# Kernel tuning notes

Measured on AMD Instinct MI355X. Metric: run time of the kernel, lower is better.

Reference implementation:

```python
import jax, jax.numpy as jnp
import numpy as np

B, T, D = 4, 4096, 1024


def setup_inputs() -> dict:
    key = jax.random.key(0)
    ks = jax.random.split(key, 7)
    s_in = 1.0 / np.sqrt(D)
    return {
        "x": jax.random.normal(ks[0], (B, T, D), dtype=jnp.float32),
        "W_in": jax.random.uniform(ks[1], (D, 2 * D), jnp.float32, -s_in, s_in),
        "b_in": jax.random.uniform(ks[2], (2 * D,), jnp.float32, -s_in, s_in),
        "A": jax.random.normal(ks[3], (D,), dtype=jnp.float32),
        "C": jax.random.normal(ks[4], (D,), dtype=jnp.float32),
        "W_out": jax.random.uniform(ks[5], (D, D), jnp.float32, -s_in, s_in),
        "b_out": jax.random.uniform(ks[6], (D,), jnp.float32, -s_in, s_in),
    }


def _ssm(v, A, C):
    # diagonal linear recurrence: h_t = sigmoid(A) * h_{t-1} + v_t ; y_t = C * h_t
    decay = jax.nn.sigmoid(A)  # (D,)
    vT = jnp.swapaxes(v, 0, 1)  # (T, B, D)

    def step(h, vt):
        h = decay * h + vt
        return h, h

    h0 = jnp.zeros(vT.shape[1:], dtype=v.dtype)
    _, hs = jax.lax.scan(step, h0, vT)  # (T, B, D)
    return jnp.swapaxes(hs, 0, 1) * C  # (B, T, D)


def reference(x, W_in, b_in, A, C, W_out, b_out):
    proj = x @ W_in + b_in  # (B, T, 2D)
    v, gate = jnp.split(proj, 2, axis=-1)
    gate = jax.nn.sigmoid(gate)
    y = gate * _ssm(v, A, C)
    return y @ W_out + b_out
```

## Files before the change

kernel.cpp:

```cpp
#include <hip/hip_runtime.h>
#include <math.h>

#define BDIM 4
#define TDIM 4096
#define DDIM 1024
#define MDIM (BDIM * TDIM)

#define NC  64
#define LCH 64
static_assert(NC * LCH == TDIM, "chunking");

typedef __attribute__((ext_vector_type(8))) short short8;
typedef __attribute__((ext_vector_type(4))) float f32x4;

__device__ __forceinline__ unsigned short f2bf(float f) {
  unsigned int u = __float_as_uint(f);
  unsigned int r = (u + 0x7fffu + ((u >> 16) & 1u)) >> 16;
  return (unsigned short)r;
}
__device__ __forceinline__ float bf2f(unsigned short h) {
  return __uint_as_float(((unsigned int)h) << 16);
}
__device__ __forceinline__ float sigmoidf_(float x) {
  return 1.0f / (1.0f + expf(-x));
}

__global__ __launch_bounds__(256) void prep_x_kernel(const float* __restrict__ x,
                                                     unsigned short* __restrict__ xh,
                                                     int n4) {
  int i = blockIdx.x * 256 + threadIdx.x;
  if (i >= n4) return;
  float4 f = ((const float4*)x)[i];
  ushort4 h;
  h.x = f2bf(f.x);
  h.y = f2bf(f.y);
  h.z = f2bf(f.z);
  h.w = f2bf(f.w);
  ((ushort4*)xh)[i] = h;
}

__global__ __launch_bounds__(256) void wprep_kernel(const float* __restrict__ in,
                                                    unsigned short* __restrict__ oh,
                                                    int K, int N) {
  __shared__ float t[64][65];
  int n0 = blockIdx.x * 64;
  int k0 = blockIdx.y * 64;
#pragma unroll
  for (int i = 0; i < 16; ++i) {
    int idx = i * 256 + threadIdx.x;
    int r = idx >> 6, c = idx & 63;
    t[r][c] = in[(size_t)(k0 + r) * N + (n0 + c)];
  }
  __syncthreads();
#pragma unroll
  for (int i = 0; i < 16; ++i) {
    int idx = i * 256 + threadIdx.x;
    int rn = idx >> 6, ck = idx & 63;
    oh[(size_t)(n0 + rn) * K + (k0 + ck)] = f2bf(t[ck][rn]);
  }
}


#define BARRIER()                                  \
  do {                                             \
    asm volatile("" ::: "memory");                 \
    __builtin_amdgcn_s_barrier();                  \
    asm volatile("" ::: "memory");                 \
  } while (0)

#define RD_A(SET, BK)                                                           \
  _Pragma("unroll") for (int m = 0; m < 4; ++m)                                 \
      SET[m] = *(const short8*)(ldsb + (((BK) ? baseA1 : baseA0) + m * 2048));

#define RD_B(SET, BK)                                                           \
  _Pragma("unroll") for (int n = 0; n < 4; ++n)                                 \
      SET[n] = *(const short8*)(ldsb + 16384 + (((BK) ? baseB1 : baseB0) +      \
                                                n * 2048));

#define MFMA16(ASET, BSET)                                                      \
  _Pragma("unroll") for (int m = 0; m < 4; ++m)                                 \
      _Pragma("unroll") for (int n = 0; n < 4; ++n)                             \
          acc[m][n] = __builtin_amdgcn_mfma_f32_16x16x32_bf16(                  \
              ASET[m], BSET[n], acc[m][n], 0, 0, 0);

#define STAGE(PTR, S, BUFB, KOFF)                                               \
  __builtin_amdgcn_global_load_lds(                                             \
      (const __attribute__((address_space(1))) unsigned int*)((PTR) + off##S +  \
                                                              (KOFF)),          \
      (__attribute__((address_space(3))) unsigned int*)((char*)lds + (BUFB) +   \
                                                        (S) * 4096 +            \
                                                        wave * 1024),           \
      16, 0, 0);

template <int EPI>
__global__ __launch_bounds__(256, 4) void gemm128(const unsigned short* __restrict__ A,
                                                  const unsigned short* __restrict__ B,
                                                  const float* __restrict__ bias,
                                                  float* __restrict__ outF,
                                                  unsigned short* __restrict__ outV,
                                                  unsigned short* __restrict__ outG,
                                                  const float* __restrict__ Adec,
                                                  float* __restrict__ chunkp,
                                                  int nNt, int K) {
  __shared__ unsigned short lds[16384];

  int cpx = gridDim.x >> 3;
  int bid = blockIdx.x;
  int swz = (bid & 7) * cpx + (bid >> 3);
  int mtile = swz / nNt, ntile = swz % nNt;

  int tid = threadIdx.x;
  int wave = tid >> 6, lane = tid & 63;
  int wm = wave >> 1, wn = wave & 1;
  int rA = wm * 64 + (lane & 15);
  int rB = wn * 64 + (lane & 15);
  int kq2 = (lane >> 4) * 16;

  int baseA0 = ((rA << 7) + kq2) ^ ((rA & 7) << 4);
  int baseA1 = ((rA << 7) + kq2 + 64) ^ ((rA & 7) << 4);
  int baseB0 = ((rB << 7) + kq2) ^ ((rB & 7) << 4);
  int baseB1 = ((rB << 7) + kq2 + 64) ^ ((rB & 7) << 4);
  const char* ldsb = (const char*)lds;

#define MKOFF(S) \
  ({ int Lt = (S) * 4096 + tid * 16; int P = Lt ^ (((Lt >> 7) & 7) << 4); \
     ((P >> 7) * (K << 1)) + (P & 127); })
  int off0 = MKOFF(0), off1 = MKOFF(1), off2 = MKOFF(2), off3 = MKOFF(3);
#undef MKOFF

  const char* AgB = (const char*)(A + (size_t)(mtile * 128) * K);
  const char* BgB = (const char*)(B + (size_t)(ntile * 128) * K);

  f32x4 acc[4][4] = {};
  short8 af[4], bf[4];

  int NT = K >> 6;
  for (int t = 0; t < NT; ++t) {
    int k0 = t << 7;
    STAGE(AgB, 0, 0, k0) STAGE(AgB, 1, 0, k0)
    STAGE(AgB, 2, 0, k0) STAGE(AgB, 3, 0, k0)
    STAGE(BgB, 0, 16384, k0) STAGE(BgB, 1, 16384, k0)
    STAGE(BgB, 2, 16384, k0) STAGE(BgB, 3, 16384, k0)
    asm volatile("s_waitcnt vmcnt(0)" ::: "memory");
    BARRIER();
    RD_A(af, 0);
    RD_B(bf, 0);
    MFMA16(af, bf);
    RD_A(af, 1);
    RD_B(bf, 1);
    MFMA16(af, bf);
    BARRIER();
  }

  int q = lane >> 4;
  int row0 = mtile * 128 + wm * 64 + (q << 2);
  int col0 = ntile * 128 + wn * 64 + (lane & 15);

  if (EPI == 0) {
#pragma unroll
    for (int m = 0; m < 4; ++m) {
#pragma unroll
      for (int n = 0; n < 4; ++n) {
        int col = col0 + n * 16;
        float bv = bias[col];
#pragma unroll
        for (int j = 0; j < 4; ++j) {
          int row = row0 + m * 16 + j;
          outF[(size_t)row * (nNt * 128) + col] = acc[m][n][j] + bv;
        }
      }
    }
  } else if (col0 >= DDIM) {
#pragma unroll
    for (int m = 0; m < 4; ++m) {
#pragma unroll
      for (int n = 0; n < 4; ++n) {
        int col = col0 + n * 16;
        float bv = bias[col];
#pragma unroll
        for (int j = 0; j < 4; ++j) {
          int row = row0 + m * 16 + j;
          outG[(size_t)row * DDIM + (col - DDIM)] = f2bf(sigmoidf_(acc[m][n][j] + bv));
        }
      }
    }
  } else {
    float partial[4];
#pragma unroll
    for (int n = 0; n < 4; ++n) {
      int col = col0 + n * 16;
      float bv = bias[col];
      float dec = sigmoidf_(Adec[col]);
      float l2d = __log2f(dec);
      float p = 0.f;
#pragma unroll
      for (int m = 0; m < 4; ++m) {
#pragma unroll
        for (int j = 0; j < 4; ++j) {
          int row = row0 + m * 16 + j;
          unsigned short ush = f2bf(acc[m][n][j] + bv);
          outV[(size_t)row * DDIM + col] = ush;
          float w = exp2f((float)(63 - (q * 4 + m * 16 + j)) * l2d);
          p = fmaf(w, bf2f(ush), p);
        }
      }
      partial[n] = p;
    }
#pragma unroll
    for (int n = 0; n < 4; ++n) {
      partial[n] += __shfl_xor(partial[n], 16, 64);
      partial[n] += __shfl_xor(partial[n], 32, 64);
    }
    if (q == 0) {
      int chunkg = mtile * 2 + wm;
#pragma unroll
      for (int n = 0; n < 4; ++n)
        chunkp[(size_t)chunkg * DDIM + col0 + n * 16] = partial[n];
    }
  }
}

__global__ __launch_bounds__(256) void ssm_phase2(const float* __restrict__ A,
                                                  const float* __restrict__ chunkp,
                                                  float* __restrict__ chunkh) {
  int idx = blockIdx.x * 256 + threadIdx.x;
  int b = idx >> 10, d = idx & 1023;
  float dec = sigmoidf_(A[d]);
  float dL = dec;
#pragma unroll
  for (int i = 0; i < 6; ++i) dL *= dL;
  float hv[NC];
#pragma unroll
  for (int c = 0; c < NC; ++c) hv[c] = chunkp[(size_t)(b * NC + c) * DDIM + d];
  float carry = 0.f;
#pragma unroll
  for (int c = 0; c < NC; ++c) {
    float local = hv[c];
    chunkh[(size_t)(b * NC + c) * DDIM + d] = carry;
    carry = fmaf(dL, carry, local);
  }
}

__global__ __launch_bounds__(256) void ssm_phase3(const unsigned short* __restrict__ v,
                                                  const unsigned short* __restrict__ g,
                                                  const float* __restrict__ A,
                                                  const float* __restrict__ C,
                                                  const float* __restrict__ chunkh,
                                                  unsigned short* __restrict__ ybf) {
  int b = blockIdx.y, c = blockIdx.x;
  int d0 = threadIdx.x * 4;
  float4 a4 = *(const float4*)&A[d0];
  float4 c4 = *(const float4*)&C[d0];
  float dx = sigmoidf_(a4.x), dy = sigmoidf_(a4.y), dz = sigmoidf_(a4.z), dw = sigmoidf_(a4.w);
  float4 h0 = *(const float4*)&chunkh[(size_t)(b * NC + c) * DDIM + d0];
  float hx = h0.x, hy = h0.y, hz = h0.z, hw = h0.w;
  size_t base = ((size_t)b * TDIM + (size_t)c * LCH) * DDIM + d0;
  const ushort4* vp = (const ushort4*)(v + base);
  const ushort4* gp = (const ushort4*)(g + base);
  ushort4* yp = (ushort4*)(ybf + base);
#pragma unroll 4
  for (int i = 0; i < LCH; ++i) {
    ushort4 vv = vp[(size_t)i * (DDIM / 4)];
    ushort4 gg = gp[(size_t)i * (DDIM / 4)];
    hx = fmaf(dx, hx, bf2f(vv.x));
    hy = fmaf(dy, hy, bf2f(vv.y));
    hz = fmaf(dz, hz, bf2f(vv.z));
    hw = fmaf(dw, hw, bf2f(vv.w));
    ushort4 yy;
    yy.x = f2bf(bf2f(gg.x) * c4.x * hx);
    yy.y = f2bf(bf2f(gg.y) * c4.y * hy);
    yy.z = f2bf(bf2f(gg.z) * c4.z * hz);
    yy.w = f2bf(bf2f(gg.w) * c4.w * hw);
    yp[(size_t)i * (DDIM / 4)] = yy;
  }
}

extern "C" void kernel_launch(void* const* d_in, const int* in_sizes, int n_in,
                              void* d_out, int out_size, void* d_ws, size_t ws_size,
                              hipStream_t stream) {
  const float* x = (const float*)d_in[0];
  const float* W_in = (const float*)d_in[1];
  const float* b_in = (const float*)d_in[2];
  const float* A = (const float*)d_in[3];
  const float* C = (const float*)d_in[4];
  const float* W_out = (const float*)d_in[5];
  const float* b_out = (const float*)d_in[6];
  float* out = (float*)d_out;

  char* ws = (char*)d_ws;
  const size_t MK = (size_t)MDIM * DDIM;
  unsigned short* xh = (unsigned short*)ws;    ws += MK * 2;
  unsigned short* winh = (unsigned short*)ws;  ws += (size_t)2 * DDIM * DDIM * 2;
  unsigned short* wouth = (unsigned short*)ws; ws += (size_t)DDIM * DDIM * 2;
  unsigned short* v = (unsigned short*)ws;     ws += MK * 2;
  unsigned short* g = (unsigned short*)ws;     ws += MK * 2;
  unsigned short* ybf = (unsigned short*)ws;   ws += MK * 2;
  float* chunkp = (float*)ws;                  ws += (size_t)BDIM * NC * DDIM * 4;
  float* chunkh = (float*)ws;                  ws += (size_t)BDIM * NC * DDIM * 4;

  prep_x_kernel<<<(int)(MK / 4 / 256), 256, 0, stream>>>(x, xh, (int)(MK / 4));
  wprep_kernel<<<dim3(2 * DDIM / 64, DDIM / 64), 256, 0, stream>>>(W_in, winh, DDIM, 2 * DDIM);
  wprep_kernel<<<dim3(DDIM / 64, DDIM / 64), 256, 0, stream>>>(W_out, wouth, DDIM, DDIM);

  gemm128<1><<<(MDIM / 128) * 16, 256, 0, stream>>>(xh, winh, b_in, nullptr, v, g,
                                                    A, chunkp, 16, DDIM);

  ssm_phase2<<<(BDIM * DDIM) / 256, 256, 0, stream>>>(A, chunkp, chunkh);
  ssm_phase3<<<dim3(NC, BDIM), 256, 0, stream>>>(v, g, A, C, chunkh, ybf);

  gemm128<0><<<(MDIM / 128) * 8, 256, 0, stream>>>(ybf, wouth, b_out, out, nullptr, nullptr,
                                                   nullptr, nullptr, 8, DDIM);
}
```

Before: 168.5 us.

## Use two-wave 128x128 GEMM tiles with 64x128 per-wave subtiles

Rewrites the GEMM block to use 128 threads (2 waves) instead of 4. Each wave now computes a 64x128 output subtile with 32 MFMA accumulators, doubling the A-fragment reuse across B columns. Global-to-LDS staging issues 8 loads per wave per operand to fill the same 128x128x64 tile. This raises per-wave register pressure and lowers the number of waves available to hide latency, since the launch bound is 2 blocks of 128 threads.

After: 174.3 us. 3.5% more time.

```diff
diff --git a/kernel.cpp b/kernel.cpp
--- a/kernel.cpp
+++ b/kernel.cpp
@@ -73,13 +73,13 @@
       SET[m] = *(const short8*)(ldsb + (((BK) ? baseA1 : baseA0) + m * 2048));
 
 #define RD_B(SET, BK)                                                           \
-  _Pragma("unroll") for (int n = 0; n < 4; ++n)                                 \
+  _Pragma("unroll") for (int n = 0; n < 8; ++n)                                 \
       SET[n] = *(const short8*)(ldsb + 16384 + (((BK) ? baseB1 : baseB0) +      \
                                                 n * 2048));
 
-#define MFMA16(ASET, BSET)                                                      \
+#define MFMA32(ASET, BSET)                                                      \
   _Pragma("unroll") for (int m = 0; m < 4; ++m)                                 \
-      _Pragma("unroll") for (int n = 0; n < 4; ++n)                             \
+      _Pragma("unroll") for (int n = 0; n < 8; ++n)                             \
           acc[m][n] = __builtin_amdgcn_mfma_f32_16x16x32_bf16(                  \
               ASET[m], BSET[n], acc[m][n], 0, 0, 0);
 
@@ -88,20 +88,26 @@
       (const __attribute__((address_space(1))) unsigned int*)((PTR) + off##S +  \
                                                               (KOFF)),          \
       (__attribute__((address_space(3))) unsigned int*)((char*)lds + (BUFB) +   \
-                                                        (S) * 4096 +            \
+                                                        (S) * 2048 +            \
                                                         wave * 1024),           \
       16, 0, 0);
 
+#define STAGE_ALL(PTR, BUFB, KOFF)                                              \
+  STAGE(PTR, 0, BUFB, KOFF) STAGE(PTR, 1, BUFB, KOFF)                           \
+  STAGE(PTR, 2, BUFB, KOFF) STAGE(PTR, 3, BUFB, KOFF)                           \
+  STAGE(PTR, 4, BUFB, KOFF) STAGE(PTR, 5, BUFB, KOFF)                           \
+  STAGE(PTR, 6, BUFB, KOFF) STAGE(PTR, 7, BUFB, KOFF)
+
 template <int EPI>
-__global__ __launch_bounds__(256, 4) void gemm128(const unsigned short* __restrict__ A,
-                                                  const unsigned short* __restrict__ B,
-                                                  const float* __restrict__ bias,
-                                                  float* __restrict__ outF,
-                                                  unsigned short* __restrict__ outV,
-                                                  unsigned short* __restrict__ outG,
-                                                  const float* __restrict__ Adec,
-                                                  float* __restrict__ chunkp,
-                                                  int nNt, int K) {
+__global__ __launch_bounds__(128, 2) void gemm128w(const unsigned short* __restrict__ A,
+                                                   const unsigned short* __restrict__ B,
+                                                   const float* __restrict__ bias,
+                                                   float* __restrict__ outF,
+                                                   unsigned short* __restrict__ outV,
+                                                   unsigned short* __restrict__ outG,
+                                                   const float* __restrict__ Adec,
+                                                   float* __restrict__ chunkp,
+                                                   int nNt, int K) {
   __shared__ unsigned short lds[16384];
 
   int cpx = gridDim.x >> 3;
@@ -111,9 +117,8 @@
 
   int tid = threadIdx.x;
   int wave = tid >> 6, lane = tid & 63;
-  int wm = wave >> 1, wn = wave & 1;
-  int rA = wm * 64 + (lane & 15);
-  int rB = wn * 64 + (lane & 15);
+  int rA = wave * 64 + (lane & 15);
+  int rB = lane & 15;
   int kq2 = (lane >> 4) * 16;
 
   int baseA0 = ((rA << 7) + kq2) ^ ((rA & 7) << 4);
@@ -123,44 +128,43 @@
   const char* ldsb = (const char*)lds;
 
 #define MKOFF(S) \
-  ({ int Lt = (S) * 4096 + tid * 16; int P = Lt ^ (((Lt >> 7) & 7) << 4); \
+  ({ int Lt = (S) * 2048 + tid * 16; int P = Lt ^ (((Lt >> 7) & 7) << 4); \
      ((P >> 7) * (K << 1)) + (P & 127); })
   int off0 = MKOFF(0), off1 = MKOFF(1), off2 = MKOFF(2), off3 = MKOFF(3);
+  int off4 = MKOFF(4), off5 = MKOFF(5), off6 = MKOFF(6), off7 = MKOFF(7);
 #undef MKOFF
 
   const char* AgB = (const char*)(A + (size_t)(mtile * 128) * K);
   const char* BgB = (const char*)(B + (size_t)(ntile * 128) * K);
 
-  f32x4 acc[4][4] = {};
-  short8 af[4], bf[4];
+  f32x4 acc[4][8] = {};
+  short8 af[4], bf[8];
 
   int NT = K >> 6;
   for (int t = 0; t < NT; ++t) {
     int k0 = t << 7;
-    STAGE(AgB, 0, 0, k0) STAGE(AgB, 1, 0, k0)
-    STAGE(AgB, 2, 0, k0) STAGE(AgB, 3, 0, k0)
-    STAGE(BgB, 0, 16384, k0) STAGE(BgB, 1, 16384, k0)
-    STAGE(BgB, 2, 16384, k0) STAGE(BgB, 3, 16384, k0)
+    STAGE_ALL(AgB, 0, k0)
+    STAGE_ALL(BgB, 16384, k0)
     asm volatile("s_waitcnt vmcnt(0)" ::: "memory");
     BARRIER();
     RD_A(af, 0);
     RD_B(bf, 0);
-    MFMA16(af, bf);
+    MFMA32(af, bf);
     RD_A(af, 1);
     RD_B(bf, 1);
-    MFMA16(af, bf);
+    MFMA32(af, bf);
     BARRIER();
   }
 
   int q = lane >> 4;
-  int row0 = mtile * 128 + wm * 64 + (q << 2);
-  int col0 = ntile * 128 + wn * 64 + (lane & 15);
+  int row0 = mtile * 128 + wave * 64 + (q << 2);
+  int col0 = ntile * 128 + (lane & 15);
 
   if (EPI == 0) {
 #pragma unroll
     for (int m = 0; m < 4; ++m) {
 #pragma unroll
-      for (int n = 0; n < 4; ++n) {
+      for (int n = 0; n < 8; ++n) {
         int col = col0 + n * 16;
         float bv = bias[col];
 #pragma unroll
@@ -174,7 +178,7 @@
 #pragma unroll
     for (int m = 0; m < 4; ++m) {
 #pragma unroll
-      for (int n = 0; n < 4; ++n) {
+      for (int n = 0; n < 8; ++n) {
         int col = col0 + n * 16;
         float bv = bias[col];
 #pragma unroll
@@ -185,9 +189,9 @@
       }
     }
   } else {
-    float partial[4];
-#pragma unroll
-    for (int n = 0; n < 4; ++n) {
+    float partial[8];
+#pragma unroll
+    for (int n = 0; n < 8; ++n) {
       int col = col0 + n * 16;
       float bv = bias[col];
       float dec = sigmoidf_(Adec[col]);
@@ -207,14 +211,14 @@
       partial[n] = p;
     }
 #pragma unroll
-    for (int n = 0; n < 4; ++n) {
+    for (int n = 0; n < 8; ++n) {
       partial[n] += __shfl_xor(partial[n], 16, 64);
       partial[n] += __shfl_xor(partial[n], 32, 64);
     }
     if (q == 0) {
-      int chunkg = mtile * 2 + wm;
-#pragma unroll
-      for (int n = 0; n < 4; ++n)
+      int chunkg = mtile * 2 + wave;
+#pragma unroll
+      for (int n = 0; n < 8; ++n)
         chunkp[(size_t)chunkg * DDIM + col0 + n * 16] = partial[n];
     }
   }
@@ -302,12 +306,12 @@
   wprep_kernel<<<dim3(2 * DDIM / 64, DDIM / 64), 256, 0, stream>>>(W_in, winh, DDIM, 2 * DDIM);
   wprep_kernel<<<dim3(DDIM / 64, DDIM / 64), 256, 0, stream>>>(W_out, wouth, DDIM, DDIM);
 
-  gemm128<1><<<(MDIM / 128) * 16, 256, 0, stream>>>(xh, winh, b_in, nullptr, v, g,
-                                                    A, chunkp, 16, DDIM);
+  gemm128w<1><<<(MDIM / 128) * 16, 128, 0, stream>>>(xh, winh, b_in, nullptr, v, g,
+                                                     A, chunkp, 16, DDIM);
 
   ssm_phase2<<<(BDIM * DDIM) / 256, 256, 0, stream>>>(A, chunkp, chunkh);
   ssm_phase3<<<dim3(NC, BDIM), 256, 0, stream>>>(v, g, A, C, chunkh, ybf);
 
-  gemm128<0><<<(MDIM / 128) * 8, 256, 0, stream>>>(ybf, wouth, b_out, out, nullptr, nullptr,
-                                                   nullptr, nullptr, 8, DDIM);
-}
+  gemm128w<0><<<(MDIM / 128) * 8, 128, 0, stream>>>(ybf, wouth, b_out, out, nullptr, nullptr,
+                                                    nullptr, nullptr, 8, DDIM);
+}
```
